# Kernel optimization log

Measured on AMD Instinct MI355X. Metric: run time of the kernel, lower is better.

The kernel has to match this reference:

```python
import jax, jax.numpy as jnp
import numpy as np

H, W = 2048, 2048          # grid shape (init arg `shape`)
N = H * W
MEAN_MODULO = 1.0


def _conv2d_valid(x, k):
    """x: [1,1,H,W], k: [3,3] fixed finite-difference kernel. Valid padding, stride 1."""
    return jax.lax.conv_general_dilated(x, k.reshape(1, 1, 3, 3), (1, 1), 'VALID')


def setup_inputs() -> dict:
    key = jax.random.key(0)
    k1, k2, k3 = jax.random.split(key, 3)
    pred_E = jax.random.uniform(k1, (N,), jnp.float32)          # E > 0 (divisor via sum conv)
    pred_v = jax.random.uniform(k2, (N,), jnp.float32)          # Poisson ratio in [0,1)
    strain = jax.random.normal(k3, (N, 3), jnp.float32)         # [exx, eyy, exy] per point
    return {"pred_E": pred_E, "pred_v": pred_v, "strain": strain}


def reference(pred_E, pred_v, strain):
    # --- calculate_stress ---
    # Original builds C(v) per row from v.detach().numpy(): the matmul part uses a
    # detached v, while the E/(1-v^2) fraction keeps gradient flow through v.
    vd = jax.lax.stop_gradient(pred_v)
    # strain[i] @ [[1,v,0],[v,1,0],[0,0,(1-v)/2]] , vectorized over all rows
    m_xx = strain[:, 0] + vd * strain[:, 1]
    m_yy = vd * strain[:, 0] + strain[:, 1]
    m_xy = strain[:, 2] * (1.0 - vd) * 0.5
    frac = pred_E / (1.0 - jnp.square(pred_v))   # gradient flows through pred_v here
    s_xx = m_xx * frac
    s_yy = m_yy * frac
    s_xy = m_xy * frac

    # --- calculate_loss_r ---
    sum_k = jnp.ones((3, 3), jnp.float32)
    wx_xx = jnp.array([[-1., -1., -1.], [0., 0., 0.], [1., 1., 1.]], jnp.float32)
    wx_xy = jnp.array([[1., 0., -1.], [1., 0., -1.], [1., 0., -1.]], jnp.float32)
    wy_yy = wx_xy   # same stencil values as in source
    wy_xy = wx_xx

    E_conv = _conv2d_valid(pred_E.reshape(1, 1, H, W), sum_k)
    fx = (_conv2d_valid(s_xx.reshape(1, 1, H, W), wx_xx)
          + _conv2d_valid(s_xy.reshape(1, 1, H, W), wx_xy))
    fy = (_conv2d_valid(s_yy.reshape(1, 1, H, W), wy_yy)
          + _conv2d_valid(s_xy.reshape(1, 1, H, W), wy_xy))

    loss_x = jnp.mean(jnp.abs(fx / E_conv))
    loss_y = jnp.mean(jnp.abs(fy / E_conv))
    loss_e = jnp.abs(jnp.mean(pred_E) - MEAN_MODULO)
    return loss_x + loss_y + loss_e / 100.0
```

## Files before the change

### kernel.cpp

```cpp
#include <hip/hip_runtime.h>

#define GH 2048
#define GW 2048
#define OH 2046
#define OW 2046

constexpr int R      = 11;
constexpr int BANDS  = 186;
constexpr int CTILES = 33;
constexpr int NWAVES = CTILES * BANDS;
constexpr int NBLOCKS = (NWAVES + 3) / 4;

__global__ __launch_bounds__(256)
void stencil_kernel(const float* __restrict__ E, const float* __restrict__ v,
                    const float* __restrict__ strain, float2* __restrict__ partials) {
    const int wid  = blockIdx.x * 4 + (threadIdx.x >> 6);
    const int lane = threadIdx.x & 63;
    if (wid >= NWAVES) return;
    const int tile = wid % CTILES;
    const int band = wid / CTILES;
    const int col  = tile * 62 + lane;
    const int row0 = band * R;

    const bool eown_col = (lane < 62) || (tile == CTILES - 1);
    const int  own_rows = (band == BANDS - 1) ? R + 2 : R;
    const bool out_ok   = (lane < 62);

    float he0=0, he1=0, he2=0, hxx0=0, hxx1=0, hxx2=0, hxy0=0, hxy1=0, hxy2=0;
    float sz0=0, sz1=0, sz2=0, sy0=0, sy1=0, sy2=0;
    float acc = 0.f, eacc = 0.f;

    int idx = row0 * GW + col;
    float e_n  = E[idx];
    float v_n  = v[idx];
    float xx_n = strain[3 * idx + 0];
    float yy_n = strain[3 * idx + 1];
    float xy_n = strain[3 * idx + 2];

    for (int k = 0; k < R + 2; ++k) {
        const float e = e_n, vv = v_n, exx = xx_n, eyy = yy_n, exy = xy_n;
        if (k < R + 1) {
            const int idx2 = idx + GW;
            e_n  = E[idx2];
            v_n  = v[idx2];
            xx_n = strain[3 * idx2 + 0];
            yy_n = strain[3 * idx2 + 1];
            xy_n = strain[3 * idx2 + 2];
        }
        if (eown_col && k < own_rows) eacc += e;

        const float frac = e / (1.f - vv * vv);
        const float sx  = (exx + vv * eyy) * frac;
        const float sy_ = (vv * exx + eyy) * frac;
        const float sz_ = exy * (1.f - vv) * 0.5f * frac;

        const float he_  = e   + __shfl_down(e,   1, 64) + __shfl_down(e,   2, 64);
        const float hxx_ = sx  + __shfl_down(sx,  1, 64) + __shfl_down(sx,  2, 64);
        const float hxy_ = sz_ + __shfl_down(sz_, 1, 64) + __shfl_down(sz_, 2, 64);

        he0 = he1;   he1 = he2;   he2 = he_;
        hxx0 = hxx1; hxx1 = hxx2; hxx2 = hxx_;
        hxy0 = hxy1; hxy1 = hxy2; hxy2 = hxy_;
        sz0 = sz1;   sz1 = sz2;   sz2 = sz_;
        sy0 = sy1;   sy1 = sy2;   sy2 = sy_;

        if (k >= 2) {
            const float Vxy = sz0 + sz1 + sz2;
            const float Vyy = sy0 + sy1 + sy2;
            const float fx = (hxx2 - hxx0) + Vxy - __shfl_down(Vxy, 2, 64);
            const float fy = (Vyy - __shfl_down(Vyy, 2, 64)) + (hxy2 - hxy0);
            const float Ec = he0 + he1 + he2;
            const float inv = 1.f / Ec;
            const float c = fabsf(fx * inv) + fabsf(fy * inv);
            acc += out_ok ? c : 0.f;
        }
        idx += GW;
    }

    #pragma unroll
    for (int off = 32; off > 0; off >>= 1) {
        acc  += __shfl_down(acc,  off, 64);
        eacc += __shfl_down(eacc, off, 64);
    }
    if (lane == 0) partials[wid] = make_float2(acc, eacc);
}

__global__ __launch_bounds__(256)
void finalize_kernel(const float2* __restrict__ partials, float* __restrict__ out) {
    __shared__ double sacc[4][2];
    double a = 0.0, e = 0.0;
    for (int i = threadIdx.x; i < NWAVES; i += 256) {
        float2 p = partials[i];
        a += (double)p.x;
        e += (double)p.y;
    }
    #pragma unroll
    for (int off = 32; off > 0; off >>= 1) {
        a += __shfl_down(a, off, 64);
        e += __shfl_down(e, off, 64);
    }
    const int wave = threadIdx.x >> 6;
    if ((threadIdx.x & 63) == 0) { sacc[wave][0] = a; sacc[wave][1] = e; }
    __syncthreads();
    if (threadIdx.x == 0) {
        double A    = sacc[0][0] + sacc[1][0] + sacc[2][0] + sacc[3][0];
        double Esum = sacc[0][1] + sacc[1][1] + sacc[2][1] + sacc[3][1];
        double M = (double)OH * (double)OW;
        double loss_xy = A / M;
        double loss_e  = fabs(Esum / ((double)GH * (double)GW) - 1.0) / 100.0;
        out[0] = (float)(loss_xy + loss_e);
    }
}

extern "C" void kernel_launch(void* const* d_in, const int* in_sizes, int n_in,
                              void* d_out, int out_size, void* d_ws, size_t ws_size,
                              hipStream_t stream) {
    const float* E      = (const float*)d_in[0];
    const float* v      = (const float*)d_in[1];
    const float* strain = (const float*)d_in[2];
    float* out = (float*)d_out;
    float2* partials = (float2*)d_ws;

    hipLaunchKernelGGL(stencil_kernel, dim3(NBLOCKS), dim3(256), 0, stream,
                       E, v, strain, partials);
    hipLaunchKernelGGL(finalize_kernel, dim3(1), dim3(256), 0, stream, partials, out);
}
```

Measured before the change: 111.5 us.

## Deepen row prefetch, double band height, precompute vertical differences, block-level partials

Each wave now covers taller bands (22 rows instead of 11), which halves the fraction of halo rows that get reloaded. A fully unrolled 3-deep register prefetch ring keeps more loads in flight. The vertical stencil terms are reformulated to shuffle raw values and accumulate differences, which drops the shuffles on the summed column values. Partials are reduced per block in shared memory, so the finalize kernel reads four times fewer entries. In exchange there are fewer waves overall (about 3069), which may lower occupancy and latency hiding, and full unrolling raises register pressure.

```diff
diff --git a/kernel.cpp b/kernel.cpp
--- a/kernel.cpp
+++ b/kernel.cpp
@@ -5,76 +5,94 @@
 #define OH 2046
 #define OW 2046
 
-constexpr int R      = 11;
-constexpr int BANDS  = 186;
-constexpr int CTILES = 33;
-constexpr int NWAVES = CTILES * BANDS;
+constexpr int R       = 22;
+constexpr int BANDS   = 93;
+constexpr int CTILES  = 33;
+constexpr int NWAVES  = CTILES * BANDS;
 constexpr int NBLOCKS = (NWAVES + 3) / 4;
+constexpr int PF      = 3;
 
 __global__ __launch_bounds__(256)
 void stencil_kernel(const float* __restrict__ E, const float* __restrict__ v,
                     const float* __restrict__ strain, float2* __restrict__ partials) {
-    const int wid  = blockIdx.x * 4 + (threadIdx.x >> 6);
-    const int lane = threadIdx.x & 63;
-    if (wid >= NWAVES) return;
-    const int tile = wid % CTILES;
-    const int band = wid / CTILES;
-    const int col  = tile * 62 + lane;
-    const int row0 = band * R;
+    const int wslot = threadIdx.x >> 6;
+    const int wid   = blockIdx.x * 4 + wslot;
+    const int lane  = threadIdx.x & 63;
 
-    const bool eown_col = (lane < 62) || (tile == CTILES - 1);
-    const int  own_rows = (band == BANDS - 1) ? R + 2 : R;
-    const bool out_ok   = (lane < 62);
-
-    float he0=0, he1=0, he2=0, hxx0=0, hxx1=0, hxx2=0, hxy0=0, hxy1=0, hxy2=0;
-    float sz0=0, sz1=0, sz2=0, sy0=0, sy1=0, sy2=0;
     float acc = 0.f, eacc = 0.f;
 
-    int idx = row0 * GW + col;
-    float e_n  = E[idx];
-    float v_n  = v[idx];
-    float xx_n = strain[3 * idx + 0];
-    float yy_n = strain[3 * idx + 1];
-    float xy_n = strain[3 * idx + 2];
+    if (wid < NWAVES) {
+        const int tile = wid % CTILES;
+        const int band = wid / CTILES;
+        const int col  = tile * 62 + lane;
+        const int row0 = band * R;
 
-    for (int k = 0; k < R + 2; ++k) {
-        const float e = e_n, vv = v_n, exx = xx_n, eyy = yy_n, exy = xy_n;
-        if (k < R + 1) {
-            const int idx2 = idx + GW;
-            e_n  = E[idx2];
-            v_n  = v[idx2];
-            xx_n = strain[3 * idx2 + 0];
-            yy_n = strain[3 * idx2 + 1];
-            xy_n = strain[3 * idx2 + 2];
+        const bool eown_col = (lane < 62) || (tile == CTILES - 1);
+        const int  own_rows = (band == BANDS - 1) ? R + 2 : R;
+        const bool out_ok   = (lane < 62);
+
+        float he0=0,he1=0,he2=0;
+        float hxx0=0,hxx1=0,hxx2=0;
+        float hxy0=0,hxy1=0,hxy2=0;
+        float dxy0=0,dxy1=0,dxy2=0;
+        float dyy0=0,dyy1=0,dyy2=0;
+
+        float eb[PF], vb[PF], xxb[PF], yyb[PF], xyb[PF];
+        int idx = row0 * GW + col;
+        #pragma unroll
+        for (int p = 0; p < PF; ++p) {
+            const int j = idx + p * GW;
+            eb[p]  = E[j];
+            vb[p]  = v[j];
+            xxb[p] = strain[3 * j + 0];
+            yyb[p] = strain[3 * j + 1];
+            xyb[p] = strain[3 * j + 2];
         }
-        if (eown_col && k < own_rows) eacc += e;
 
-        const float frac = e / (1.f - vv * vv);
-        const float sx  = (exx + vv * eyy) * frac;
-        const float sy_ = (vv * exx + eyy) * frac;
-        const float sz_ = exy * (1.f - vv) * 0.5f * frac;
+        #pragma unroll
+        for (int k = 0; k < R + 2; ++k) {
+            const int s = k % PF;
+            const float e   = eb[s];
+            const float vv  = vb[s];
+            const float exx = xxb[s];
+            const float eyy = yyb[s];
+            const float exy = xyb[s];
+            if (k + PF < R + 2) {
+                const int j = idx + PF * GW;
+                eb[s]  = E[j];
+                vb[s]  = v[j];
+                xxb[s] = strain[3 * j + 0];
+                yyb[s] = strain[3 * j + 1];
+                xyb[s] = strain[3 * j + 2];
+            }
+            idx += GW;
 
-        const float he_  = e   + __shfl_down(e,   1, 64) + __shfl_down(e,   2, 64);
-        const float hxx_ = sx  + __shfl_down(sx,  1, 64) + __shfl_down(sx,  2, 64);
-        const float hxy_ = sz_ + __shfl_down(sz_, 1, 64) + __shfl_down(sz_, 2, 64);
+            if (eown_col && k < own_rows) eacc += e;
 
-        he0 = he1;   he1 = he2;   he2 = he_;
-        hxx0 = hxx1; hxx1 = hxx2; hxx2 = hxx_;
-        hxy0 = hxy1; hxy1 = hxy2; hxy2 = hxy_;
-        sz0 = sz1;   sz1 = sz2;   sz2 = sz_;
-        sy0 = sy1;   sy1 = sy2;   sy2 = sy_;
+            const float frac = e / (1.f - vv * vv);
+            const float sx  = (exx + vv * eyy) * frac;
+            const float sy_ = (vv * exx + eyy) * frac;
+            const float sz_ = exy * (1.f - vv) * 0.5f * frac;
 
-        if (k >= 2) {
-            const float Vxy = sz0 + sz1 + sz2;
-            const float Vyy = sy0 + sy1 + sy2;
-            const float fx = (hxx2 - hxx0) + Vxy - __shfl_down(Vxy, 2, 64);
-            const float fy = (Vyy - __shfl_down(Vyy, 2, 64)) + (hxy2 - hxy0);
-            const float Ec = he0 + he1 + he2;
-            const float inv = 1.f / Ec;
-            const float c = fabsf(fx * inv) + fabsf(fy * inv);
-            acc += out_ok ? c : 0.f;
+            const float e1 = __shfl_down(e,   1, 64), e2 = __shfl_down(e,   2, 64);
+            const float x1 = __shfl_down(sx,  1, 64), x2 = __shfl_down(sx,  2, 64);
+            const float z1 = __shfl_down(sz_, 1, 64), z2 = __shfl_down(sz_, 2, 64);
+            const float y2 = __shfl_down(sy_, 2, 64);
+
+            he0=he1;   he1=he2;   he2  = e   + e1 + e2;
+            hxx0=hxx1; hxx1=hxx2; hxx2 = sx  + x1 + x2;
+            hxy0=hxy1; hxy1=hxy2; hxy2 = sz_ + z1 + z2;
+            dxy0=dxy1; dxy1=dxy2; dxy2 = sz_ - z2;
+            dyy0=dyy1; dyy1=dyy2; dyy2 = sy_ - y2;
+
+            if (k >= 2) {
+                const float fx = (hxx2 - hxx0) + (dxy0 + dxy1 + dxy2);
+                const float fy = (dyy0 + dyy1 + dyy2) + (hxy2 - hxy0);
+                const float inv = 1.f / (he0 + he1 + he2);
+                const float c = fabsf(fx * inv) + fabsf(fy * inv);
+                acc += out_ok ? c : 0.f;
+            }
         }
-        idx += GW;
     }
 
     #pragma unroll
@@ -82,14 +100,22 @@
         acc  += __shfl_down(acc,  off, 64);
         eacc += __shfl_down(eacc, off, 64);
     }
-    if (lane == 0) partials[wid] = make_float2(acc, eacc);
+    __shared__ float sred[4][2];
+    if (lane == 0) { sred[wslot][0] = acc; sred[wslot][1] = eacc; }
+    __syncthreads();
+    if (threadIdx.x == 0) {
+        partials[blockIdx.x] =
+            make_float2(sred[0][0] + sred[1][0] + sred[2][0] + sred[3][0],
+                        sred[0][1] + sred[1][1] + sred[2][1] + sred[3][1]);
+    }
 }
 
 __global__ __launch_bounds__(256)
 void finalize_kernel(const float2* __restrict__ partials, float* __restrict__ out) {
     __shared__ double sacc[4][2];
     double a = 0.0, e = 0.0;
-    for (int i = threadIdx.x; i < NWAVES; i += 256) {
+    #pragma unroll
+    for (int i = threadIdx.x; i < NBLOCKS; i += 256) {
         float2 p = partials[i];
         a += (double)p.x;
         e += (double)p.y;
```

Result: slower. 116.0 us (+4.1%).
